# Performance work log

Hardware: AMD Instinct MI355X
Metric: run time of the kernel (lower is better)

The kernel has to match this reference:

```python
import jax, jax.numpy as jnp
import numpy as np

N = 50000
E = 400000
NF = 320
HID = 320
EPS = 1e-08


def _linear(x, W, b=None):
    y = x @ W.T
    return y if b is None else y + b


def setup_inputs() -> dict:
    key = jax.random.key(0)
    ks = jax.random.split(key, 16)
    s = 0.05
    inp = {
        "h": jax.random.normal(ks[0], (N, NF), jnp.float32),
        "coord": jax.random.normal(ks[1], (N, 3), jnp.float32),
        "edge_index": jax.random.randint(ks[2], (2, E), 0, N, jnp.int32),
        # edge_mlp: Linear(2*NF+1 -> HID), SiLU, Linear(HID -> HID), SiLU
        "W_e1": jax.random.normal(ks[3], (HID, 2 * NF + 1), jnp.float32) * s,
        "b_e1": jnp.zeros((HID,), jnp.float32),
        "W_e2": jax.random.normal(ks[4], (HID, HID), jnp.float32) * s,
        "b_e2": jnp.zeros((HID,), jnp.float32),
        # node_mlp: Linear(HID+NF -> HID), SiLU, Linear(HID -> NF)
        "W_n1": jax.random.normal(ks[5], (HID, HID + NF), jnp.float32) * s,
        "b_n1": jnp.zeros((HID,), jnp.float32),
        "W_n2": jax.random.normal(ks[6], (NF, HID), jnp.float32) * s,
        "b_n2": jnp.zeros((NF,), jnp.float32),
        # coord_mlp: Linear(HID -> HID), SiLU, Linear(HID -> 1, no bias, xavier gain .001)
        "W_c1": jax.random.normal(ks[7], (HID, HID), jnp.float32) * s,
        "b_c1": jnp.zeros((HID,), jnp.float32),
        "W_c2": jax.random.normal(ks[8], (1, HID), jnp.float32) * 0.001,
    }
    return inp


def reference(h, coord, edge_index, W_e1, b_e1, W_e2, b_e2,
              W_n1, b_n1, W_n2, b_n2, W_c1, b_c1, W_c2):
    row, col = edge_index[0], edge_index[1]

    # coord2radial (normalize=True hard-coded in the module)
    coord_diff = coord[row] - coord[col]                      # [E,3]
    radial = jnp.sum(coord_diff ** 2, axis=1, keepdims=True)  # [E,1]
    norm = jax.lax.stop_gradient(jnp.sqrt(radial)) + EPS
    coord_diff = coord_diff / norm

    # edge model: gather endpoint feats, MLP with SiLU
    edge_in = jnp.concatenate([h[row], h[col], radial], axis=1)   # [E, 2*NF+1]
    m = jax.nn.silu(_linear(edge_in, W_e1, b_e1))
    m = jax.nn.silu(_linear(m, W_e2, b_e2))                       # [E, HID]

    # coord model: per-edge scalar weight, scatter-sum to nodes
    w = _linear(jax.nn.silu(_linear(m, W_c1, b_c1)), W_c2)        # [E,1]
    trans = coord_diff * w                                        # [E,3]
    coord_agg = jax.ops.segment_sum(trans, row, num_segments=N)   # [N,3]
    coord_out = coord + coord_agg

    # node model: scatter-sum messages, MLP, residual
    agg = jax.ops.segment_sum(m, row, num_segments=N)             # [N,HID]
    node_in = jnp.concatenate([h, agg], axis=1)                   # [N,HID+NF]
    out = _linear(jax.nn.silu(_linear(node_in, W_n1, b_n1)), W_n2, b_n2)
    h_out = h + out

    return (h_out, coord_out)
```

## Files before the change

kernel.cpp:

```cpp
#include <hip/hip_runtime.h>

#define NN 50000
#define NE 400000
#define NFD 320
#define NB1 196

typedef short bf16x8 __attribute__((ext_vector_type(8)));
typedef float f32x4 __attribute__((ext_vector_type(4)));

#define MFMA16 __builtin_amdgcn_mfma_f32_16x16x32_bf16

__device__ __forceinline__ unsigned short f2bf(float f){
  unsigned int u = __float_as_uint(f);
  u += 0x7fffu + ((u >> 16) & 1u);
  return (unsigned short)(u >> 16);
}
__device__ __forceinline__ unsigned int cvt_pk_bf16(float lo, float hi){
  unsigned int r;
  asm("v_cvt_pk_bf16_f32 %0, %1, %2" : "=v"(r) : "v"(lo), "v"(hi));
  return r;
}
__device__ __forceinline__ float bflo(unsigned int q){ return __uint_as_float(q << 16); }
__device__ __forceinline__ float bfhi(unsigned int q){ return __uint_as_float(q & 0xffff0000u); }
__device__ __forceinline__ float rcp_fast(float x){
  float r;
  asm("v_rcp_f32 %0, %1" : "=v"(r) : "v"(x));
  return r;
}
__device__ __forceinline__ float silu_f(float x){
  return x * rcp_fast(1.f + __expf(-x));
}

__device__ __forceinline__ void pack_w_body(const float* __restrict__ W,
                                            unsigned short* __restrict__ P,
                                            int kstride, int KS, int idx){
  if (idx >= 20 * KS * 64) return;
  int lane = idx & 63;
  int t  = idx >> 6;
  int ks = t % KS;
  int ct = t / KS;
  const float* src = W + (size_t)(ct*16 + (lane & 15)) * kstride + ks*32 + 8*(lane >> 4);
  unsigned int q[4];
  #pragma unroll
  for (int j = 0; j < 4; j++) q[j] = cvt_pk_bf16(src[2*j], src[2*j+1]);
  *(uint4*)(P + (size_t)idx * 8) = make_uint4(q[0], q[1], q[2], q[3]);
}

__device__ __forceinline__ void pack_stack_body(const float* __restrict__ We1,
                                                unsigned short* __restrict__ P, int idx){
  if (idx >= 40 * 10 * 64) return;
  int lane = idx & 63;
  int t  = idx >> 6;
  int ks = t % 10;
  int ct = t / 10;
  int o  = ct*16 + (lane & 15);
  int k  = ks*32 + 8*(lane >> 4);
  const float* src = (o < 320) ? (We1 + (size_t)o * 641 + k)
                               : (We1 + (size_t)(o - 320) * 641 + 320 + k);
  unsigned int q[4];
  #pragma unroll
  for (int j = 0; j < 4; j++) q[j] = cvt_pk_bf16(src[2*j], src[2*j+1]);
  *(uint4*)(P + (size_t)idx * 8) = make_uint4(q[0], q[1], q[2], q[3]);
}

#define PREP_PACK_B 176
#define PREP_CIN_B  293
#define PREP_HIST_B 782
__global__ void __launch_bounds__(512)
prep_k(const float* __restrict__ We2, const float* __restrict__ Wc1,
       const float* __restrict__ Wn1, const float* __restrict__ Wn2,
       const float* __restrict__ We1,
       unsigned short* __restrict__ We2p, unsigned short* __restrict__ Wc1p,
       unsigned short* __restrict__ Wn1p, unsigned short* __restrict__ Wn2p,
       unsigned short* __restrict__ Wsp, float* __restrict__ we1l,
       const float* __restrict__ coord, float* __restrict__ outc,
       const int* __restrict__ ei, int* __restrict__ cnt){
  int b = blockIdx.x;
  int tid = threadIdx.x;
  if (b < PREP_PACK_B){
    int idx = b*512 + tid;
    if (idx < 12800)       pack_w_body(We2, We2p, 320, 10, idx);
    else if (idx < 25600)  pack_w_body(Wc1, Wc1p, 320, 10, idx - 12800);
    else if (idx < 51200)  pack_w_body(Wn1, Wn1p, 640, 20, idx - 25600);
    else if (idx < 64000)  pack_w_body(Wn2, Wn2p, 320, 10, idx - 51200);
    else if (idx < 89600)  pack_stack_body(We1, Wsp, idx - 64000);
    else if (idx < 89920){
      int o = idx - 89600;
      we1l[o] = We1[(size_t)o * 641 + 640];
    }
  } else if (b < PREP_PACK_B + PREP_CIN_B){
    int i = (b - PREP_PACK_B)*512 + tid;
    if (i < NN*3) outc[i] = coord[i];
  } else {
    int e = (b - PREP_PACK_B - PREP_CIN_B)*512 + tid;
    if (e < NE) atomicAdd(&cnt[ei[e]], 1);
  }
}

__global__ void scan1(const int* __restrict__ cnt, int* __restrict__ cur,
                      int* __restrict__ bsum){
  __shared__ int sh[256];
  int tid = threadIdx.x;
  int i = blockIdx.x * 256 + tid;
  int v = (i < NN) ? cnt[i] : 0;
  sh[tid] = v;
  __syncthreads();
  for (int d = 1; d < 256; d <<= 1){
    int u = (tid >= d) ? sh[tid - d] : 0;
    __syncthreads();
    sh[tid] += u;
    __syncthreads();
  }
  if (i < NN) cur[i] = sh[tid] - v;
  if (tid == 255) bsum[blockIdx.x] = sh[255];
}

__global__ void scan2(int* __restrict__ bsum){
  __shared__ int sh[256];
  int tid = threadIdx.x;
  int v = (tid < NB1) ? bsum[tid] : 0;
  sh[tid] = v;
  __syncthreads();
  for (int d = 1; d < 256; d <<= 1){
    int u = (tid >= d) ? sh[tid - d] : 0;
    __syncthreads();
    sh[tid] += u;
    __syncthreads();
  }
  if (tid < NB1) bsum[tid] = sh[tid] - v;
}

__global__ void scan3(int* __restrict__ cur, const int* __restrict__ bsum){
  int i = blockIdx.x * 256 + threadIdx.x;
  if (i < NN) cur[i] += bsum[blockIdx.x];
}

__device__ __forceinline__ void gemm5(const unsigned short* __restrict__ s,
                                      const unsigned short* __restrict__ wp,
                                      int arow0, int arow1, int kl,
                                      int fragbase, int KST, int lane, f32x4 (&acc)[2][5]){
  const unsigned short* wl0 = wp + (size_t)fragbase * 512 + (size_t)lane * 8;
  bf16x8 b0[5], b1[5];
  #pragma unroll
  for (int t = 0; t < 5; t++) b0[t] = *(const bf16x8*)(wl0 + (t*KST + 0)*512);
  #pragma unroll
  for (int t = 0; t < 5; t++) b1[t] = *(const bf16x8*)(wl0 + (t*KST + 1)*512);
  #pragma unroll
  for (int ks = 0; ks < 10; ks++){
    bf16x8 a0 = *(const bf16x8*)(s + arow0*328 + ks*32 + kl);
    bf16x8 a1 = *(const bf16x8*)(s + arow1*328 + ks*32 + kl);
    bf16x8 cur[5];
    #pragma unroll
    for (int t = 0; t < 5; t++) cur[t] = (ks & 1) ? b1[t] : b0[t];
    if (ks < 8){
      #pragma unroll
      for (int t = 0; t < 5; t++){
        bf16x8 nv = *(const bf16x8*)(wl0 + (t*KST + ks + 2)*512);
        if (ks & 1) b1[t] = nv; else b0[t] = nv;
      }
    }
    #pragma unroll
    for (int t = 0; t < 5; t++){
      acc[0][t] = MFMA16(a0, cur[t], acc[0][t], 0, 0, 0);
      acc[1][t] = MFMA16(a1, cur[t], acc[1][t], 0, 0, 0);
    }
  }
}

#define SP_SCAT_B 782
__global__ void __launch_bounds__(512, 4)
scat_pre(const int* __restrict__ ei, int* __restrict__ cur, int* __restrict__ perm,
         const float* __restrict__ h, const unsigned short* __restrict__ Wsp,
         const float* __restrict__ be1, unsigned short* __restrict__ P){
  if (blockIdx.x < SP_SCAT_B){
    int e = blockIdx.x * 512 + threadIdx.x;
    if (e < NE){
      int p = atomicAdd(&cur[ei[e]], 1);
      perm[p] = e;
    }
    return;
  }
  __shared__ __align__(16) unsigned short s_h[32*328];

  const int tid  = threadIdx.x;
  const int lane = tid & 63;
  const int ch   = tid >> 6;
  const int n0   = (blockIdx.x - SP_SCAT_B) * 32;

  const int arow0 = (lane & 15);
  const int arow1 = 16 + (lane & 15);
  const int kl = 8 * (lane >> 4);
  const int rb = (lane >> 4) * 4;

  #pragma unroll
  for (int i = 0; i < 5; i++){
    int idx = tid + i*512;
    int r = idx / 80;
    int c = idx - r*80;
    int node = n0 + r;
    float4 v = (node < NN) ? *(const float4*)(h + (size_t)node*NFD + c*4)
                           : make_float4(0,0,0,0);
    *(uint2*)(s_h + r*328 + c*4) = make_uint2(cvt_pk_bf16(v.x, v.y), cvt_pk_bf16(v.z, v.w));
  }
  __syncthreads();

  f32x4 acc[2][5];
  #pragma unroll
  for (int rt = 0; rt < 2; rt++)
    #pragma unroll
    for (int t = 0; t < 5; t++) acc[rt][t] = {0.f,0.f,0.f,0.f};

  gemm5(s_h, Wsp, arow0, arow1, kl, ch*50, 10, lane, acc);

  #pragma unroll
  for (int rt = 0; rt < 2; rt++){
    #pragma unroll
    for (int t = 0; t < 5; t++){
      int o = (ch*5 + t)*16 + (lane & 15);
      float bb = (o < 320) ? be1[o] : 0.f;
      #pragma unroll
      for (int r = 0; r < 4; r++){
        int node = n0 + rt*16 + rb + r;
        if (node < NN) P[(size_t)node*640 + o] = f2bf(acc[rt][t][r] + bb);
      }
    }
  }
}

#define EDGE_NWG (NE/32)
#define SWZ_Q (EDGE_NWG/8)
#define SWZ_R (EDGE_NWG%8)
__global__ void __launch_bounds__(256, 5)
edge_kernel(const unsigned short* __restrict__ Pbf, const float* __restrict__ coord,
            const int* __restrict__ ei, const int* __restrict__ perm,
            const float* __restrict__ we1l,
            const unsigned short* __restrict__ We2p, const float* __restrict__ be2,
            const unsigned short* __restrict__ Wc1p, const float* __restrict__ bc1,
            const float* __restrict__ Wc2,
            unsigned short* __restrict__ agg, float* __restrict__ cacc)
{
  __shared__ __align__(16) unsigned short s_b[32*328];
  __shared__ float4 s_cd[32];
  __shared__ int s_row[32];
  __shared__ int s_col[32];
  __shared__ float s_w[32];

  const int tid  = threadIdx.x;
  const int lane = tid & 63;
  const int ch   = tid >> 6;

  const int orig = blockIdx.x;
  const int xcd  = orig & 7;
  const int k    = orig >> 3;
  const int wgid = (xcd < SWZ_R ? xcd*(SWZ_Q+1) : SWZ_R*(SWZ_Q+1) + (xcd-SWZ_R)*SWZ_Q) + k;
  const int e0   = wgid * 32;

  if (tid < 32){
    int e = perm[e0 + tid];
    int r = ei[e];
    int c = ei[NE + e];
    s_row[tid] = r; s_col[tid] = c;
    s_w[tid] = 0.f;
    float dx = coord[r*3+0] - coord[c*3+0];
    float dy = coord[r*3+1] - coord[c*3+1];
    float dz = coord[r*3+2] - coord[c*3+2];
    float rad = dx*dx + dy*dy + dz*dz;
    float inv = 1.f / (sqrtf(rad) + 1e-8f);
    s_cd[tid] = make_float4(dx*inv, dy*inv, dz*inv, rad);
  }
  __syncthreads();

  const int arow0 = (lane & 15);
  const int arow1 = 16 + (lane & 15);
  const int kl = 8 * (lane >> 4);
  const int rb = (lane >> 4) * 4;

  #pragma unroll
  for (int i = 0; i < 5; i++){
    int idx = tid + i*256;
    int r = idx / 40;
    int c = idx - r*40;
    uint4 pr = *(const uint4*)(Pbf + (size_t)s_row[r]*640 + c*8);
    uint4 pc = *(const uint4*)(Pbf + (size_t)s_col[r]*640 + 320 + c*8);
    float4 wA = *(const float4*)(we1l + c*8);
    float4 wB = *(const float4*)(we1l + c*8 + 4);
    float rad = s_cd[r].w;
    float v0 = silu_f(bflo(pr.x) + bflo(pc.x) + rad*wA.x);
    float v1 = silu_f(bfhi(pr.x) + bfhi(pc.x) + rad*wA.y);
    float v2 = silu_f(bflo(pr.y) + bflo(pc.y) + rad*wA.z);
    float v3 = silu_f(bfhi(pr.y) + bfhi(pc.y) + rad*wA.w);
    float v4 = silu_f(bflo(pr.z) + bflo(pc.z) + rad*wB.x);
    float v5 = silu_f(bfhi(pr.z) + bfhi(pc.z) + rad*wB.y);
    float v6 = silu_f(bflo(pr.w) + bflo(pc.w) + rad*wB.z);
    float v7 = silu_f(bfhi(pr.w) + bfhi(pc.w) + rad*wB.w);
    uint4 q;
    q.x = cvt_pk_bf16(v0, v1);
    q.y = cvt_pk_bf16(v2, v3);
    q.z = cvt_pk_bf16(v4, v5);
    q.w = cvt_pk_bf16(v6, v7);
    *(uint4*)(s_b + r*328 + c*8) = q;
  }
  __syncthreads();

  f32x4 acc[2][5];

  #pragma unroll
  for (int rt = 0; rt < 2; rt++)
    #pragma unroll
    for (int t = 0; t < 5; t++) acc[rt][t] = {0.f,0.f,0.f,0.f};
  gemm5(s_b, We2p, arow0, arow1, kl, ch*50, 10, lane, acc);
  __syncthreads();
  #pragma unroll
  for (int t = 0; t < 5; t++){
    int o = (ch*5 + t)*16 + (lane & 15);
    float bb = be2[o];
    #pragma unroll
    for (int r = 0; r < 4; r++){
      float v0 = silu_f(acc[0][t][r] + bb);
      float v1 = silu_f(acc[1][t][r] + bb);
      unsigned int q = cvt_pk_bf16(v0, v1);
      int er = rb + r;
      s_b[er*328 + o] = (unsigned short)q;
      s_b[(er+16)*328 + o] = (unsigned short)(q >> 16);
    }
  }
  __syncthreads();

  #pragma unroll
  for (int rt = 0; rt < 2; rt++)
    #pragma unroll
    for (int t = 0; t < 5; t++) acc[rt][t] = {0.f,0.f,0.f,0.f};
  gemm5(s_b, Wc1p, arow0, arow1, kl, ch*50, 10, lane, acc);
  {
    float part[2][4];
    #pragma unroll
    for (int rt = 0; rt < 2; rt++)
      #pragma unroll
      for (int r = 0; r < 4; r++) part[rt][r] = 0.f;
    #pragma unroll
    for (int t = 0; t < 5; t++){
      int o = (ch*5 + t)*16 + (lane & 15);
      float bb = bc1[o];
      float wc = Wc2[o];
      #pragma unroll
      for (int rt = 0; rt < 2; rt++)
        #pragma unroll
        for (int r = 0; r < 4; r++)
          part[rt][r] = fmaf(silu_f(acc[rt][t][r] + bb), wc, part[rt][r]);
    }
    #pragma unroll
    for (int rt = 0; rt < 2; rt++)
      #pragma unroll
      for (int r = 0; r < 4; r++){
        float p = part[rt][r];
        p += __shfl_xor(p, 1);
        p += __shfl_xor(p, 2);
        p += __shfl_xor(p, 4);
        p += __shfl_xor(p, 8);
        if ((lane & 15) == 0)
          atomicAdd(&s_w[rt*16 + (lane >> 4)*4 + r], p);
      }
  }
  __syncthreads();

  if (tid < 160){
    int p = tid;
    float a0 = 0.f, a1 = 0.f;
    #pragma unroll
    for (int e = 0; e < 32; e++){
      unsigned int q = *(const unsigned int*)(s_b + e*328 + p*2);
      a0 += bflo(q); a1 += bfhi(q);
      if (e == 31 || s_row[e+1] != s_row[e]){
        unsigned int val = cvt_pk_bf16(a0, a1);
        unsigned short* dst = agg + (size_t)s_row[e]*NFD + p*2;
        asm volatile("global_atomic_pk_add_bf16 %0, %1, off" :: "v"(dst), "v"(val) : "memory");
        a0 = 0.f; a1 = 0.f;
      }
    }
  }
  if (tid >= 192 && tid < 195){
    int d = tid - 192;
    float a = 0.f;
    #pragma unroll
    for (int e = 0; e < 32; e++){
      float cdc = (d == 0) ? s_cd[e].x : (d == 1) ? s_cd[e].y : s_cd[e].z;
      a += cdc * s_w[e];
      if (e == 31 || s_row[e+1] != s_row[e]){
        atomicAdd(cacc + (size_t)s_row[e]*3 + d, a);
        a = 0.f;
      }
    }
  }
}

__global__ void __launch_bounds__(512, 4)
node_kernel(const float* __restrict__ h, const unsigned short* __restrict__ agg,
            const unsigned short* __restrict__ Wn1p, const float* __restrict__ bn1,
            const unsigned short* __restrict__ Wn2p, const float* __restrict__ bn2,
            float* __restrict__ hout)
{
  __shared__ __align__(16) unsigned short s_b[64*328];

  const int tid  = threadIdx.x;
  const int lane = tid & 63;
  const int wv   = tid >> 6;
  const int ch   = wv & 3;
  const int rh   = wv >> 2;
  const int n0   = blockIdx.x * 64;

  const int arow0 = rh*32 + (lane & 15);
  const int arow1 = rh*32 + 16 + (lane & 15);
  const int kl = 8 * (lane >> 4);
  const int rb = (lane >> 4) * 4;

  f32x4 acc[2][5];
  #pragma unroll
  for (int rt = 0; rt < 2; rt++)
    #pragma unroll
    for (int t = 0; t < 5; t++) acc[rt][t] = {0.f,0.f,0.f,0.f};

  #pragma unroll
  for (int i = 0; i < 10; i++){
    int idx = tid + i*512;
    int r = idx / 80;
    int c = idx - r*80;
    int node = n0 + r;
    float4 v = (node < NN) ? *(const float4*)(h + (size_t)node*NFD + c*4)
                           : make_float4(0,0,0,0);
    *(uint2*)(s_b + r*328 + c*4) = make_uint2(cvt_pk_bf16(v.x, v.y), cvt_pk_bf16(v.z, v.w));
  }
  __syncthreads();

  gemm5(s_b, Wn1p, arow0, arow1, kl, ch*100, 20, lane, acc);
  __syncthreads();

  #pragma unroll
  for (int i = 0; i < 5; i++){
    int idx = tid + i*512;
    int r = idx / 40;
    int c = idx - r*40;
    int node = n0 + r;
    uint4 v = (node < NN) ? *(const uint4*)(agg + (size_t)node*NFD + c*8)
                          : make_uint4(0,0,0,0);
    *(uint4*)(s_b + r*328 + c*8) = v;
  }
  __syncthreads();

  gemm5(s_b, Wn1p, arow0, arow1, kl, ch*100 + 10, 20, lane, acc);
  __syncthreads();

  #pragma unroll
  for (int t = 0; t < 5; t++){
    int o = (ch*5 + t)*16 + (lane & 15);
    float bb = bn1[o];
    #pragma unroll
    for (int r = 0; r < 4; r++){
      float v0 = silu_f(acc[0][t][r] + bb);
      float v1 = silu_f(acc[1][t][r] + bb);
      unsigned int q = cvt_pk_bf16(v0, v1);
      int er = rh*32 + rb + r;
      s_b[er*328 + o] = (unsigned short)q;
      s_b[(er+16)*328 + o] = (unsigned short)(q >> 16);
    }
  }
  __syncthreads();

  #pragma unroll
  for (int rt = 0; rt < 2; rt++)
    #pragma unroll
    for (int t = 0; t < 5; t++) acc[rt][t] = {0.f,0.f,0.f,0.f};
  gemm5(s_b, Wn2p, arow0, arow1, kl, ch*50, 10, lane, acc);
  #pragma unroll
  for (int t = 0; t < 5; t++){
    int o = (ch*5 + t)*16 + (lane & 15);
    float bb = bn2[o];
    #pragma unroll
    for (int r = 0; r < 4; r++){
      int node0 = n0 + rh*32 + rb + r;
      int node1 = node0 + 16;
      if (node0 < NN)
        hout[(size_t)node0*NFD + o] = h[(size_t)node0*NFD + o] + acc[0][t][r] + bb;
      if (node1 < NN)
        hout[(size_t)node1*NFD + o] = h[(size_t)node1*NFD + o] + acc[1][t][r] + bb;
    }
  }
}

extern "C" void kernel_launch(void* const* d_in, const int* in_sizes, int n_in,
                              void* d_out, int out_size, void* d_ws, size_t ws_size,
                              hipStream_t stream){
  const float* h     = (const float*)d_in[0];
  const float* coord = (const float*)d_in[1];
  const int*   ei    = (const int*)d_in[2];
  const float* We1 = (const float*)d_in[3];
  const float* be1 = (const float*)d_in[4];
  const float* We2 = (const float*)d_in[5];
  const float* be2 = (const float*)d_in[6];
  const float* Wn1 = (const float*)d_in[7];
  const float* bn1 = (const float*)d_in[8];
  const float* Wn2 = (const float*)d_in[9];
  const float* bn2 = (const float*)d_in[10];
  const float* Wc1 = (const float*)d_in[11];
  const float* bc1 = (const float*)d_in[12];
  const float* Wc2 = (const float*)d_in[13];

  char* ws = (char*)d_ws;
  unsigned short* We2p = (unsigned short*)(ws);
  unsigned short* Wc1p = (unsigned short*)(ws + 204800);
  unsigned short* Wn1p = (unsigned short*)(ws + 409600);
  unsigned short* Wn2p = (unsigned short*)(ws + 819200);
  unsigned short* Wsp  = (unsigned short*)(ws + 1024000);
  float*          we1l = (float*)(ws + 1433600);
  unsigned short* agg  = (unsigned short*)(ws + 1434880);
  int*            cnt  = (int*)(ws + 33434880);
  int*            cur  = (int*)(ws + 33634880);
  int*            perm = (int*)(ws + 33834880);
  int*            bsum = (int*)(ws + 35434880);

  float* hout = (float*)d_out;
  float* cout = hout + (size_t)NN * NFD;
  unsigned short* Pbf = (unsigned short*)d_out;

  hipMemsetAsync(agg, 0, (size_t)NN * NFD * 2, stream);
  hipMemsetAsync(cnt, 0, (size_t)NN * 4, stream);

  prep_k<<<PREP_PACK_B + PREP_CIN_B + PREP_HIST_B, 512, 0, stream>>>(
      We2, Wc1, Wn1, Wn2, We1, We2p, Wc1p, Wn1p, Wn2p, Wsp, we1l,
      coord, cout, ei, cnt);

  scan1<<<NB1, 256, 0, stream>>>(cnt, cur, bsum);
  scan2<<<1, 256, 0, stream>>>(bsum);
  scan3<<<NB1, 256, 0, stream>>>(cur, bsum);

  scat_pre<<<SP_SCAT_B + (NN + 31)/32, 512, 0, stream>>>(
      ei, cur, perm, h, Wsp, be1, Pbf);

  edge_kernel<<<EDGE_NWG, 256, 0, stream>>>(Pbf, coord, ei, perm, we1l,
                                            We2p, be2, Wc1p, bc1, Wc2, agg, cout);
  node_kernel<<<(NN + 63)/64, 512, 0, stream>>>(h, agg, Wn1p, bn1, Wn2p, bn2, hout);
}
```

Baseline: 533.7 us.

## Process two 32-edge tiles per edge block with register-prefetched gathers

Each edge workgroup now handles 64 edges as two 32-edge halves with separate LDS buffers. The second half's gathered P rows are loaded into registers alongside the first half's gathers, and the two halves' GEMM, SiLU and scatter stages are interleaved. The aim is to hide gather latency behind MFMA work and to amortise per-block setup. This costs much higher register pressure from the prefetch arrays and twice the LDS per block. Launch-bounds occupancy drops from 5 to 3, and the XCD-aware block swizzle is removed.

```diff
diff --git a/kernel.cpp b/kernel.cpp
--- a/kernel.cpp
+++ b/kernel.cpp
@@ -227,10 +227,7 @@
   }
 }
 
-#define EDGE_NWG (NE/32)
-#define SWZ_Q (EDGE_NWG/8)
-#define SWZ_R (EDGE_NWG%8)
-__global__ void __launch_bounds__(256, 5)
+__global__ void __launch_bounds__(256, 3)
 edge_kernel(const unsigned short* __restrict__ Pbf, const float* __restrict__ coord,
             const int* __restrict__ ei, const int* __restrict__ perm,
             const float* __restrict__ we1l,
@@ -239,23 +236,19 @@
             const float* __restrict__ Wc2,
             unsigned short* __restrict__ agg, float* __restrict__ cacc)
 {
-  __shared__ __align__(16) unsigned short s_b[32*328];
-  __shared__ float4 s_cd[32];
-  __shared__ int s_row[32];
-  __shared__ int s_col[32];
-  __shared__ float s_w[32];
+  __shared__ __align__(16) unsigned short s_b0[32*328];
+  __shared__ __align__(16) unsigned short s_b1[32*328];
+  __shared__ float4 s_cd[64];
+  __shared__ int s_row[64];
+  __shared__ int s_col[64];
+  __shared__ float s_w[64];
 
   const int tid  = threadIdx.x;
   const int lane = tid & 63;
   const int ch   = tid >> 6;
-
-  const int orig = blockIdx.x;
-  const int xcd  = orig & 7;
-  const int k    = orig >> 3;
-  const int wgid = (xcd < SWZ_R ? xcd*(SWZ_Q+1) : SWZ_R*(SWZ_Q+1) + (xcd-SWZ_R)*SWZ_Q) + k;
-  const int e0   = wgid * 32;
-
-  if (tid < 32){
+  const int e0   = blockIdx.x * 64;
+
+  if (tid < 64){
     int e = perm[e0 + tid];
     int r = ei[e];
     int c = ei[NE + e];
@@ -275,6 +268,10 @@
   const int kl = 8 * (lane >> 4);
   const int rb = (lane >> 4) * 4;
 
+  const int gr = tid / 40;
+
+  uint4 PR1[5], PC1[5];
+
   #pragma unroll
   for (int i = 0; i < 5; i++){
     int idx = tid + i*256;
@@ -282,6 +279,8 @@
     int c = idx - r*40;
     uint4 pr = *(const uint4*)(Pbf + (size_t)s_row[r]*640 + c*8);
     uint4 pc = *(const uint4*)(Pbf + (size_t)s_col[r]*640 + 320 + c*8);
+    PR1[i] = *(const uint4*)(Pbf + (size_t)s_row[32 + r]*640 + c*8);
+    PC1[i] = *(const uint4*)(Pbf + (size_t)s_col[32 + r]*640 + 320 + c*8);
     float4 wA = *(const float4*)(we1l + c*8);
     float4 wB = *(const float4*)(we1l + c*8 + 4);
     float rad = s_cd[r].w;
@@ -298,7 +297,7 @@
     q.y = cvt_pk_bf16(v2, v3);
     q.z = cvt_pk_bf16(v4, v5);
     q.w = cvt_pk_bf16(v6, v7);
-    *(uint4*)(s_b + r*328 + c*8) = q;
+    *(uint4*)(s_b0 + r*328 + c*8) = q;
   }
   __syncthreads();
 
@@ -308,7 +307,7 @@
   for (int rt = 0; rt < 2; rt++)
     #pragma unroll
     for (int t = 0; t < 5; t++) acc[rt][t] = {0.f,0.f,0.f,0.f};
-  gemm5(s_b, We2p, arow0, arow1, kl, ch*50, 10, lane, acc);
+  gemm5(s_b0, We2p, arow0, arow1, kl, ch*50, 10, lane, acc);
   __syncthreads();
   #pragma unroll
   for (int t = 0; t < 5; t++){
@@ -320,9 +319,35 @@
       float v1 = silu_f(acc[1][t][r] + bb);
       unsigned int q = cvt_pk_bf16(v0, v1);
       int er = rb + r;
-      s_b[er*328 + o] = (unsigned short)q;
-      s_b[(er+16)*328 + o] = (unsigned short)(q >> 16);
-    }
+      s_b0[er*328 + o] = (unsigned short)q;
+      s_b0[(er+16)*328 + o] = (unsigned short)(q >> 16);
+    }
+  }
+
+  #pragma unroll
+  for (int i = 0; i < 5; i++){
+    int idx = tid + i*256;
+    int r = idx / 40;
+    int c = idx - r*40;
+    uint4 pr = PR1[i];
+    uint4 pc = PC1[i];
+    float4 wA = *(const float4*)(we1l + c*8);
+    float4 wB = *(const float4*)(we1l + c*8 + 4);
+    float rad = s_cd[32 + r].w;
+    float v0 = silu_f(bflo(pr.x) + bflo(pc.x) + rad*wA.x);
+    float v1 = silu_f(bfhi(pr.x) + bfhi(pc.x) + rad*wA.y);
+    float v2 = silu_f(bflo(pr.y) + bflo(pc.y) + rad*wA.z);
+    float v3 = silu_f(bfhi(pr.y) + bfhi(pc.y) + rad*wA.w);
+    float v4 = silu_f(bflo(pr.z) + bflo(pc.z) + rad*wB.x);
+    float v5 = silu_f(bfhi(pr.z) + bfhi(pc.z) + rad*wB.y);
+    float v6 = silu_f(bflo(pr.w) + bflo(pc.w) + rad*wB.z);
+    float v7 = silu_f(bfhi(pr.w) + bfhi(pc.w) + rad*wB.w);
+    uint4 q;
+    q.x = cvt_pk_bf16(v0, v1);
+    q.y = cvt_pk_bf16(v2, v3);
+    q.z = cvt_pk_bf16(v4, v5);
+    q.w = cvt_pk_bf16(v6, v7);
+    *(uint4*)(s_b1 + r*328 + c*8) = q;
   }
   __syncthreads();
 
@@ -330,7 +355,7 @@
   for (int rt = 0; rt < 2; rt++)
     #pragma unroll
     for (int t = 0; t < 5; t++) acc[rt][t] = {0.f,0.f,0.f,0.f};
-  gemm5(s_b, Wc1p, arow0, arow1, kl, ch*50, 10, lane, acc);
+  gemm5(s_b0, Wc1p, arow0, arow1, kl, ch*50, 10, lane, acc);
   {
     float part[2][4];
     #pragma unroll
@@ -361,14 +386,34 @@
           atomicAdd(&s_w[rt*16 + (lane >> 4)*4 + r], p);
       }
   }
-  __syncthreads();
+
+  #pragma unroll
+  for (int rt = 0; rt < 2; rt++)
+    #pragma unroll
+    for (int t = 0; t < 5; t++) acc[rt][t] = {0.f,0.f,0.f,0.f};
+  gemm5(s_b1, We2p, arow0, arow1, kl, ch*50, 10, lane, acc);
+  __syncthreads();
+  #pragma unroll
+  for (int t = 0; t < 5; t++){
+    int o = (ch*5 + t)*16 + (lane & 15);
+    float bb = be2[o];
+    #pragma unroll
+    for (int r = 0; r < 4; r++){
+      float v0 = silu_f(acc[0][t][r] + bb);
+      float v1 = silu_f(acc[1][t][r] + bb);
+      unsigned int q = cvt_pk_bf16(v0, v1);
+      int er = rb + r;
+      s_b1[er*328 + o] = (unsigned short)q;
+      s_b1[(er+16)*328 + o] = (unsigned short)(q >> 16);
+    }
+  }
 
   if (tid < 160){
     int p = tid;
     float a0 = 0.f, a1 = 0.f;
     #pragma unroll
     for (int e = 0; e < 32; e++){
-      unsigned int q = *(const unsigned int*)(s_b + e*328 + p*2);
+      unsigned int q = *(const unsigned int*)(s_b0 + e*328 + p*2);
       a0 += bflo(q); a1 += bfhi(q);
       if (e == 31 || s_row[e+1] != s_row[e]){
         unsigned int val = cvt_pk_bf16(a0, a1);
@@ -386,6 +431,75 @@
       float cdc = (d == 0) ? s_cd[e].x : (d == 1) ? s_cd[e].y : s_cd[e].z;
       a += cdc * s_w[e];
       if (e == 31 || s_row[e+1] != s_row[e]){
+        atomicAdd(cacc + (size_t)s_row[e]*3 + d, a);
+        a = 0.f;
+      }
+    }
+  }
+  __syncthreads();
+
+  #pragma unroll
+  for (int rt = 0; rt < 2; rt++)
+    #pragma unroll
+    for (int t = 0; t < 5; t++) acc[rt][t] = {0.f,0.f,0.f,0.f};
+  gemm5(s_b1, Wc1p, arow0, arow1, kl, ch*50, 10, lane, acc);
+  {
+    float part[2][4];
+    #pragma unroll
+    for (int rt = 0; rt < 2; rt++)
+      #pragma unroll
+      for (int r = 0; r < 4; r++) part[rt][r] = 0.f;
+    #pragma unroll
+    for (int t = 0; t < 5; t++){
+      int o = (ch*5 + t)*16 + (lane & 15);
+      float bb = bc1[o];
+      float wc = Wc2[o];
+      #pragma unroll
+      for (int rt = 0; rt < 2; rt++)
+        #pragma unroll
+        for (int r = 0; r < 4; r++)
+          part[rt][r] = fmaf(silu_f(acc[rt][t][r] + bb), wc, part[rt][r]);
+    }
+    #pragma unroll
+    for (int rt = 0; rt < 2; rt++)
+      #pragma unroll
+      for (int r = 0; r < 4; r++){
+        float p = part[rt][r];
+        p += __shfl_xor(p, 1);
+        p += __shfl_xor(p, 2);
+        p += __shfl_xor(p, 4);
+        p += __shfl_xor(p, 8);
+        if ((lane & 15) == 0)
+          atomicAdd(&s_w[32 + rt*16 + (lane >> 4)*4 + r], p);
+      }
+  }
+  __syncthreads();
+
+  if (tid < 160){
+    int p = tid;
+    float a0 = 0.f, a1 = 0.f;
+    #pragma unroll
+    for (int k = 0; k < 32; k++){
+      int e = 32 + k;
+      unsigned int q = *(const unsigned int*)(s_b1 + k*328 + p*2);
+      a0 += bflo(q); a1 += bfhi(q);
+      if (k == 31 || s_row[e+1] != s_row[e]){
+        unsigned int val = cvt_pk_bf16(a0, a1);
+        unsigned short* dst = agg + (size_t)s_row[e]*NFD + p*2;
+        asm volatile("global_atomic_pk_add_bf16 %0, %1, off" :: "v"(dst), "v"(val) : "memory");
+        a0 = 0.f; a1 = 0.f;
+      }
+    }
+  }
+  if (tid >= 192 && tid < 195){
+    int d = tid - 192;
+    float a = 0.f;
+    #pragma unroll
+    for (int k = 0; k < 32; k++){
+      int e = 32 + k;
+      float cdc = (d == 0) ? s_cd[e].x : (d == 1) ? s_cd[e].y : s_cd[e].z;
+      a += cdc * s_w[e];
+      if (k == 31 || s_row[e+1] != s_row[e]){
         atomicAdd(cacc + (size_t)s_row[e]*3 + d, a);
         a = 0.f;
       }
@@ -535,7 +649,7 @@
   scat_pre<<<SP_SCAT_B + (NN + 31)/32, 512, 0, stream>>>(
       ei, cur, perm, h, Wsp, be1, Pbf);
 
-  edge_kernel<<<EDGE_NWG, 256, 0, stream>>>(Pbf, coord, ei, perm, we1l,
-                                            We2p, be2, Wc1p, bc1, Wc2, agg, cout);
+  edge_kernel<<<NE/64, 256, 0, stream>>>(Pbf, coord, ei, perm, we1l,
+                                         We2p, be2, Wc1p, bc1, Wc2, agg, cout);
   node_kernel<<<(NN + 63)/64, 512, 0, stream>>>(h, agg, Wn1p, bn1, Wn2p, bn2, hout);
 }
```

Result: slower. 703.9 us (+31.9%).
